# Kernel tuning notes

Measured on AMD Instinct MI355X. Metric: run time of the kernel, lower is better.

## Reference

```python
import jax, jax.numpy as jnp
import numpy as np

EPS = 1e-06
N_HEADS = 32
HEAD_DIM = 128
D_STATE = 128
D_MODEL = 2048
D_INNER = 4096
BATCH = 64


def setup_inputs() -> dict:
    key = jax.random.key(0)
    ks = jax.random.split(key, 8)
    bc_dim = N_HEADS * D_STATE
    theta_dim = N_HEADS * (D_STATE // 2)
    proj_dim = 2 * D_INNER + 2 * bc_dim + 2 * N_HEADS + theta_dim  # 18496
    x = jax.random.normal(ks[0], (BATCH, D_MODEL), jnp.float32)
    h = jax.random.normal(ks[1], (BATCH, N_HEADS, D_STATE, HEAD_DIM), jnp.float32) * 0.1
    B_prev = jax.random.normal(ks[2], (BATCH, N_HEADS, D_STATE), jnp.float32)
    x_prev = jax.random.normal(ks[3], (BATCH, N_HEADS, HEAD_DIM), jnp.float32)
    theta_cumsum = jax.random.normal(ks[4], (BATCH, N_HEADS, D_STATE // 2), jnp.float32)
    W_in = jax.random.normal(ks[5], (proj_dim, D_MODEL), jnp.float32) * 0.02
    # A_log initialized as log(arange(1, d_state+1)) repeated per head
    A_log = jnp.log(jnp.arange(1, D_STATE + 1, dtype=jnp.float32))[None, :].repeat(N_HEADS, axis=0)
    B_bias = jnp.ones((N_HEADS, D_STATE), jnp.float32)
    C_bias = jnp.ones((N_HEADS, D_STATE), jnp.float32)
    W_out = jax.random.normal(ks[6], (D_MODEL, D_INNER), jnp.float32) * 0.02
    return {"x": x, "h": h, "B_prev": B_prev, "x_prev": x_prev,
            "theta_cumsum": theta_cumsum, "W_in": W_in, "A_log": A_log,
            "B_bias": B_bias, "C_bias": C_bias, "W_out": W_out}


def _rms_norm(v):
    # RMS over last dim (v already fp32)
    rms = jnp.sqrt(jnp.mean(v * v, axis=-1, keepdims=True) + EPS)
    return v / rms


def _apply_rope(v, freqs):
    # v: (B,H,N), freqs: (B,H,N//2); interleaved pairs
    vp = v.reshape(*v.shape[:-1], -1, 2)
    c, s = jnp.cos(freqs), jnp.sin(freqs)
    v0, v1 = vp[..., 0], vp[..., 1]
    y0 = v0 * c - v1 * s
    y1 = v0 * s + v1 * c
    return jnp.stack([y0, y1], axis=-1).reshape(v.shape)


def reference(x, h, B_prev, x_prev, theta_cumsum, W_in, A_log, B_bias, C_bias, W_out):
    batch = x.shape[0]
    bc_dim = N_HEADS * D_STATE
    proj = x @ W_in.T  # (B, proj_dim)
    idx = 0
    x_proj = proj[:, idx:idx + D_INNER]; idx += D_INNER
    z = proj[:, idx:idx + D_INNER]; idx += D_INNER
    B_raw = proj[:, idx:idx + bc_dim]; idx += bc_dim
    C_raw = proj[:, idx:idx + bc_dim]; idx += bc_dim
    dt_raw = proj[:, idx:idx + N_HEADS]; idx += N_HEADS
    lam_raw = proj[:, idx:idx + N_HEADS]; idx += N_HEADS
    theta = proj[:, idx:].reshape(batch, N_HEADS, D_STATE // 2)

    x_proj = x_proj.reshape(batch, N_HEADS, HEAD_DIM)
    z = z.reshape(batch, N_HEADS, HEAD_DIM)
    B_raw = B_raw.reshape(batch, N_HEADS, D_STATE)
    C_raw = C_raw.reshape(batch, N_HEADS, D_STATE)

    B = _rms_norm(B_raw) + B_bias
    C = _rms_norm(C_raw) + C_bias

    dt = jax.nn.softplus(dt_raw)                       # (B,H)
    theta_cumsum_new = theta_cumsum + theta * dt[:, :, None]
    B = _apply_rope(B, theta_cumsum_new)
    C = _apply_rope(C, theta_cumsum_new)

    lam = jax.nn.sigmoid(lam_raw)                      # (B,H)
    A = -jnp.mean(jnp.exp(A_log), axis=-1)             # (H,)
    alpha = jnp.exp(dt * A)                            # (B,H)
    beta = (1.0 - lam) * dt * alpha
    gamma = lam * dt

    Bx_prev = jnp.einsum('bhn,bhp->bhnp', B_prev, x_prev)
    Bx_curr = jnp.einsum('bhn,bhp->bhnp', B, x_proj)
    h_new = (alpha[:, :, None, None] * h
             + beta[:, :, None, None] * Bx_prev
             + gamma[:, :, None, None] * Bx_curr)      # (B,H,N,P)

    y = jnp.einsum('bhn,bhnp->bhp', C, h_new)
    y = y * jax.nn.silu(z)
    y = y.reshape(batch, D_INNER) @ W_out.T            # (B, d_model)
    return y, h_new, B, x_proj, theta_cumsum_new
```

## Files before the change

kernel.cpp:

```cpp
#include <hip/hip_runtime.h>
#include <hip/hip_bf16.h>
#include <cstdint>
#include <cmath>

#define EPSV 1e-6f
#define PSTR 1183744

typedef __attribute__((ext_vector_type(8))) short bf16x8;
typedef __attribute__((ext_vector_type(4))) float f32x4;

typedef __attribute__((address_space(3))) unsigned int lds_u32;
typedef const __attribute__((address_space(1))) unsigned int g_u32;

__device__ __forceinline__ void load_lds16(const void* g, void* l) {
  __builtin_amdgcn_global_load_lds((g_u32*)g, (lds_u32*)l, 16, 0, 0);
}

__device__ __forceinline__ short f2b(float f) {
  unsigned u = __float_as_uint(f);
  u = (u + 0x7fffu + ((u >> 16) & 1u)) >> 16;
  return (short)u;
}

__device__ __forceinline__ bf16x8 cvt8(float4 a, float4 b) {
  bf16x8 v;
  v[0]=f2b(a.x); v[1]=f2b(a.y); v[2]=f2b(a.z); v[3]=f2b(a.w);
  v[4]=f2b(b.x); v[5]=f2b(b.y); v[6]=f2b(b.z); v[7]=f2b(b.w);
  return v;
}

__global__ __launch_bounds__(256) void conv_bf16(
    const float* __restrict__ in, short* __restrict__ out, int n8) {
  const int i = blockIdx.x * 256 + threadIdx.x;
  if (i < n8) {
    float4 a = ((const float4*)in)[2 * i];
    float4 b = ((const float4*)in)[2 * i + 1];
    ((bf16x8*)out)[i] = cvt8(a, b);
  }
}

#define GLOAD4(dst, base) \
  asm volatile("global_load_dwordx4 %0, %1, off" : "=&v"(dst) : "v"(base) : "memory")
#define GLOAD4O(dst, base, OFF) \
  asm volatile("global_load_dwordx4 %0, %1, off offset:" #OFF \
               : "=&v"(dst) : "v"(base) : "memory")

template<int KSPLIT, int NCHUNK>
__global__ __launch_bounds__(256, 4) void gemm_alds(
    const short* __restrict__ Abf, const float* __restrict__ W,
    float* __restrict__ Outp, int N, int K) {
  __shared__ short Alds[64 * 256];
  const int tid = threadIdx.x;
  const int lane = tid & 63;
  const int wv = tid >> 6;
  const int lrow = lane & 15, lk = lane >> 4;
  const int bid = blockIdx.x;
  const int ks = bid % KSPLIT;
  const int n0 = (bid / KSPLIT) * 64 + wv * 16;
  const int kbase = ks * (NCHUNK * 256);

  f32x4 acc[4];
#pragma unroll
  for (int i = 0; i < 4; ++i) acc[i] = (f32x4){0.f, 0.f, 0.f, 0.f};

  const int sr = (lane >> 5);
  const int ss = lane & 31;

  float4 wbuf[2][2];

#define WISSUE(B, CH, T) do { \
    const float* wp_ = W + (size_t)(n0 + lrow) * K + kbase + (CH) * 256 + (T) * 32 + lk * 8; \
    GLOAD4 (wbuf[B][0], wp_); \
    GLOAD4O(wbuf[B][1], wp_, 16); \
  } while (0)

#pragma unroll
  for (int ch = 0; ch < NCHUNK; ++ch) {
    __builtin_amdgcn_s_barrier();
#pragma unroll
    for (int j = 0; j < 8; ++j) {
      const int c = wv * 8 + j;
      const int r = 2 * c + sr;
      const int g = ss ^ (r & 31);
      load_lds16(Abf + (size_t)r * K + kbase + ch * 256 + g * 8,
                 (char*)Alds + c * 1024);
    }
    WISSUE(0, ch, 0);
    asm volatile("s_waitcnt vmcnt(2)" ::: "memory");
    __builtin_amdgcn_sched_barrier(0);
    __builtin_amdgcn_s_barrier();

#pragma unroll
    for (int t = 0; t < 8; ++t) {
      if (t < 7) {
        WISSUE((t + 1) & 1, ch, t + 1);
        asm volatile("s_waitcnt vmcnt(2)" ::: "memory");
      } else {
        asm volatile("s_waitcnt vmcnt(0)" ::: "memory");
      }
      __builtin_amdgcn_sched_barrier(0);
      const bf16x8 wb = cvt8(wbuf[t & 1][0], wbuf[t & 1][1]);
#pragma unroll
      for (int mf = 0; mf < 4; ++mf) {
        const int rm = mf * 16 + lrow;
        const int s = (t * 4 + lk) ^ (rm & 31);
        const bf16x8 av = *(const bf16x8*)((const char*)Alds + rm * 512 + s * 16);
        acc[mf] = __builtin_amdgcn_mfma_f32_16x16x32_bf16(av, wb, acc[mf], 0, 0, 0);
      }
    }
  }
#undef WISSUE

  float* ob = Outp + (size_t)ks * 64 * N + n0 + lrow;
#pragma unroll
  for (int mf = 0; mf < 4; ++mf)
#pragma unroll
    for (int i = 0; i < 4; ++i)
      ob[(size_t)(mf * 16 + lk * 4 + i) * N] = acc[mf][i];
}

__device__ __forceinline__ float block_reduce_sum256(float v, float* red, int t) {
#pragma unroll
  for (int o = 32; o > 0; o >>= 1) v += __shfl_xor(v, o, 64);
  __syncthreads();
  if ((t & 63) == 0) red[t >> 6] = v;
  __syncthreads();
  return red[0] + red[1] + red[2] + red[3];
}

__global__ __launch_bounds__(256) void state_update(
    const float* __restrict__ pp, const float* __restrict__ h,
    const float* __restrict__ B_prev, const float* __restrict__ x_prev,
    const float* __restrict__ theta_cumsum, const float* __restrict__ A_log,
    const float* __restrict__ B_bias, const float* __restrict__ C_bias,
    float* __restrict__ o_h, float* __restrict__ o_B,
    float* __restrict__ o_xp, float* __restrict__ o_th,
    short* __restrict__ ysbf) {
  const int bid = blockIdx.x;
  const int b = bid >> 5, hd = bid & 31;
  const int t = threadIdx.x;
  const size_t pb = (size_t)b * 18496;
#define PJ(o) (pp[pb + (o)] + pp[PSTR + pb + (o)] + pp[2 * PSTR + pb + (o)] \
             + pp[3 * PSTR + pb + (o)])

  __shared__ float sB[128], sC[128], sBp[128], sXp[128], sXv[128];
  __shared__ float red[8];
  __shared__ float yred[8][128];

  float aval = (t < 128) ? expf(A_log[hd * 128 + t]) : 0.f;
  float brv  = (t < 128) ? PJ(8192 + hd * 128 + t) : 0.f;
  float crv  = (t < 128) ? PJ(12288 + hd * 128 + t) : 0.f;
  if (t < 128) {
    sBp[t] = B_prev[(size_t)bid * 128 + t];
    float xp = PJ(hd * 128 + t);
    sXp[t] = xp;
    o_xp[(size_t)bid * 128 + t] = xp;
    sXv[t] = x_prev[(size_t)bid * 128 + t];
  }
  float sumA  = block_reduce_sum256(aval, red, t);
  float sumB2 = block_reduce_sum256(brv * brv, red, t);
  float sumC2 = block_reduce_sum256(crv * crv, red, t);

  const float dt_raw  = PJ(16384 + hd);
  const float lam_raw = PJ(16416 + hd);
  const float dt  = (dt_raw > 20.f) ? dt_raw : log1pf(expf(dt_raw));
  const float lam = 1.f / (1.f + expf(-lam_raw));
  const float A     = -sumA * (1.f / 128.f);
  const float alpha = expf(dt * A);
  const float beta  = (1.f - lam) * dt * alpha;
  const float gamma = lam * dt;
  const float rb = rsqrtf(sumB2 * (1.f / 128.f) + EPSV);
  const float rc = rsqrtf(sumC2 * (1.f / 128.f) + EPSV);

  if (t < 64) {
    float b0 = PJ(8192 + hd * 128 + 2 * t);
    float b1 = PJ(8192 + hd * 128 + 2 * t + 1);
    float c0 = PJ(12288 + hd * 128 + 2 * t);
    float c1 = PJ(12288 + hd * 128 + 2 * t + 1);
    b0 = b0 * rb + B_bias[hd * 128 + 2 * t];
    b1 = b1 * rb + B_bias[hd * 128 + 2 * t + 1];
    c0 = c0 * rc + C_bias[hd * 128 + 2 * t];
    c1 = c1 * rc + C_bias[hd * 128 + 2 * t + 1];
    const float th = theta_cumsum[(size_t)bid * 64 + t]
                   + PJ(16448 + hd * 64 + t) * dt;
    o_th[(size_t)bid * 64 + t] = th;
    const float cth = cosf(th), sth = sinf(th);
    const float nb0 = b0 * cth - b1 * sth, nb1 = b0 * sth + b1 * cth;
    const float nc0 = c0 * cth - c1 * sth, nc1 = c0 * sth + c1 * cth;
    sB[2 * t] = nb0; sB[2 * t + 1] = nb1;
    sC[2 * t] = nc0; sC[2 * t + 1] = nc1;
    o_B[(size_t)bid * 128 + 2 * t] = nb0;
    o_B[(size_t)bid * 128 + 2 * t + 1] = nb1;
  }
  __syncthreads();

  const int p4 = t & 31, nb = t >> 5;
  const float4 xp4 = *(const float4*)&sXp[p4 * 4];
  const float4 xv4 = *(const float4*)&sXv[p4 * 4];
  const size_t hbase = (size_t)bid * 16384;
  float4 ya = {0.f, 0.f, 0.f, 0.f};
  for (int n = nb; n < 128; n += 8) {
    const float4 hv = *(const float4*)&h[hbase + n * 128 + p4 * 4];
    const float cb = gamma * sB[n];
    const float cp = beta * sBp[n];
    float4 hn;
    hn.x = alpha * hv.x + cp * xv4.x + cb * xp4.x;
    hn.y = alpha * hv.y + cp * xv4.y + cb * xp4.y;
    hn.z = alpha * hv.z + cp * xv4.z + cb * xp4.z;
    hn.w = alpha * hv.w + cp * xv4.w + cb * xp4.w;
    *(float4*)&o_h[hbase + n * 128 + p4 * 4] = hn;
    const float cn = sC[n];
    ya.x += cn * hn.x; ya.y += cn * hn.y; ya.z += cn * hn.z; ya.w += cn * hn.w;
  }
  *(float4*)&yred[nb][p4 * 4] = ya;
  __syncthreads();
  if (t < 128) {
    float y = 0.f;
#pragma unroll
    for (int j = 0; j < 8; ++j) y += yred[j][t];
    const float zv = PJ(4096 + hd * 128 + t);
    const float sig = 1.f / (1.f + expf(-zv));
    ysbf[(size_t)b * 4096 + hd * 128 + t] = f2b(y * zv * sig);
  }
#undef PJ
}

__global__ __launch_bounds__(256) void reduce_y(
    const float* __restrict__ yp, float* __restrict__ y, int n4) {
  const int i = blockIdx.x * 256 + threadIdx.x;
  if (i < n4) {
    float4 s = ((const float4*)yp)[i];
#pragma unroll
    for (int k = 1; k < 16; ++k) {
      float4 t = ((const float4*)(yp + (size_t)k * 131072))[i];
      s.x += t.x; s.y += t.y; s.z += t.z; s.w += t.w;
    }
    ((float4*)y)[i] = s;
  }
}

extern "C" void kernel_launch(void* const* d_in, const int* in_sizes, int n_in,
                              void* d_out, int out_size, void* d_ws, size_t ws_size,
                              hipStream_t stream) {
  const float* x            = (const float*)d_in[0];
  const float* h            = (const float*)d_in[1];
  const float* B_prev       = (const float*)d_in[2];
  const float* x_prev       = (const float*)d_in[3];
  const float* theta_cumsum = (const float*)d_in[4];
  const float* W_in         = (const float*)d_in[5];
  const float* A_log        = (const float*)d_in[6];
  const float* B_bias       = (const float*)d_in[7];
  const float* C_bias       = (const float*)d_in[8];
  const float* W_out        = (const float*)d_in[9];

  float* out  = (float*)d_out;
  float* o_y  = out;
  float* o_h  = out + 131072;
  float* o_B  = o_h + 33554432;
  float* o_xp = o_B + 262144;
  float* o_th = o_xp + 262144;

  float* pp   = (float*)d_ws;
  float* yp   = pp;
  short* xbf  = (short*)(pp + 4 * PSTR);
  short* ysbf = xbf + 131072;

  conv_bf16<<<dim3(64), dim3(256), 0, stream>>>(x, xbf, 16384);
  gemm_alds<4, 2><<<dim3(289 * 4), dim3(256), 0, stream>>>(
      xbf, W_in, pp, 18496, 2048);
  state_update<<<dim3(2048), dim3(256), 0, stream>>>(
      pp, h, B_prev, x_prev, theta_cumsum, A_log, B_bias, C_bias,
      o_h, o_B, o_xp, o_th, ysbf);
  gemm_alds<16, 1><<<dim3(32 * 16), dim3(256), 0, stream>>>(
      ysbf, W_out, yp, 2048, 4096);
  reduce_y<<<dim3(128), dim3(256), 0, stream>>>(yp, o_y, 32768);
}
```

Measured before the change: 124.6 us.

## Stage W and A tiles through LDS with triple-buffered async pipeline

Rewrites the GEMM kernel so that both the fp32 weight tiles and the bf16 activation tiles go through LDS via global_load_lds. The K loop runs in 64-wide steps with a three-deep buffer ring and a prefetch distance of two. Previously A was loaded into LDS once per 256-wide chunk while W went straight into registers with a two-step prefetch. The aim is to keep more memory traffic in flight, since the weight stream is the main cost. In exchange LDS use per block rises, occupancy drops to 2 blocks per CU, and there is a barrier on every 64-wide K step.

```diff
diff --git a/kernel.cpp b/kernel.cpp
--- a/kernel.cpp
+++ b/kernel.cpp
@@ -39,79 +39,79 @@
   }
 }
 
-#define GLOAD4(dst, base) \
-  asm volatile("global_load_dwordx4 %0, %1, off" : "=&v"(dst) : "v"(base) : "memory")
-#define GLOAD4O(dst, base, OFF) \
-  asm volatile("global_load_dwordx4 %0, %1, off offset:" #OFF \
-               : "=&v"(dst) : "v"(base) : "memory")
-
-template<int KSPLIT, int NCHUNK>
-__global__ __launch_bounds__(256, 4) void gemm_alds(
+template<int KSPLIT, int NT>
+__global__ __launch_bounds__(256, 2) void gemm_wlds(
     const short* __restrict__ Abf, const float* __restrict__ W,
     float* __restrict__ Outp, int N, int K) {
-  __shared__ short Alds[64 * 256];
+  __shared__ float Wlds[3][64 * 64];
+  __shared__ short Alds[3][64 * 64];
   const int tid = threadIdx.x;
   const int lane = tid & 63;
   const int wv = tid >> 6;
   const int lrow = lane & 15, lk = lane >> 4;
   const int bid = blockIdx.x;
   const int ks = bid % KSPLIT;
-  const int n0 = (bid / KSPLIT) * 64 + wv * 16;
-  const int kbase = ks * (NCHUNK * 256);
+  const int nblk = (bid / KSPLIT) * 64;
+  const int kbase = ks * (NT * 64);
 
   f32x4 acc[4];
 #pragma unroll
   for (int i = 0; i < 4; ++i) acc[i] = (f32x4){0.f, 0.f, 0.f, 0.f};
 
-  const int sr = (lane >> 5);
-  const int ss = lane & 31;
-
-  float4 wbuf[2][2];
-
-#define WISSUE(B, CH, T) do { \
-    const float* wp_ = W + (size_t)(n0 + lrow) * K + kbase + (CH) * 256 + (T) * 32 + lk * 8; \
-    GLOAD4 (wbuf[B][0], wp_); \
-    GLOAD4O(wbuf[B][1], wp_, 16); \
-  } while (0)
-
-#pragma unroll
-  for (int ch = 0; ch < NCHUNK; ++ch) {
-    __builtin_amdgcn_s_barrier();
-#pragma unroll
-    for (int j = 0; j < 8; ++j) {
-      const int c = wv * 8 + j;
-      const int r = 2 * c + sr;
-      const int g = ss ^ (r & 31);
-      load_lds16(Abf + (size_t)r * K + kbase + ch * 256 + g * 8,
-                 (char*)Alds + c * 1024);
-    }
-    WISSUE(0, ch, 0);
-    asm volatile("s_waitcnt vmcnt(2)" ::: "memory");
+  auto stage = [&](int buf, int k0) {
+#pragma unroll
+    for (int j = 0; j < 4; ++j) {
+      const int c = wv * 4 + j;
+      const int r = c * 4 + (lane >> 4);
+      const int g = (lane & 15) ^ (r & 15);
+      load_lds16(W + (size_t)(nblk + r) * K + k0 + g * 4,
+                 (char*)&Wlds[buf][0] + c * 1024);
+    }
+#pragma unroll
+    for (int j = 0; j < 2; ++j) {
+      const int c = wv * 2 + j;
+      const int r = c * 8 + (lane >> 3);
+      const int g = (lane & 7) ^ (r & 7);
+      load_lds16(Abf + (size_t)r * K + k0 + g * 8,
+                 (char*)&Alds[buf][0] + c * 1024);
+    }
+  };
+
+  auto compute = [&](int buf) {
+    const int wr = wv * 16 + lrow;
+#pragma unroll
+    for (int kc = 0; kc < 2; ++kc) {
+      const int g0 = kc * 8 + lk * 2;
+      const float4 wlo = *(const float4*)((const char*)&Wlds[buf][0]
+                          + wr * 256 + ((g0 ^ (lrow & 15)) * 16));
+      const float4 whi = *(const float4*)((const char*)&Wlds[buf][0]
+                          + wr * 256 + (((g0 + 1) ^ (lrow & 15)) * 16));
+      const bf16x8 wb = cvt8(wlo, whi);
+#pragma unroll
+      for (int mf = 0; mf < 4; ++mf) {
+        const int ar = mf * 16 + lrow;
+        const int ga = ((kc << 2) | lk) ^ (ar & 7);
+        const bf16x8 av = *(const bf16x8*)((const char*)&Alds[buf][0]
+                           + ar * 128 + ga * 16);
+        acc[mf] = __builtin_amdgcn_mfma_f32_16x16x32_bf16(av, wb, acc[mf], 0, 0, 0);
+      }
+    }
+  };
+
+  stage(0, kbase);
+  stage(1, kbase + 64);
+
+  for (int t = 0; t < NT; ++t) {
+    if (t < NT - 1) asm volatile("s_waitcnt vmcnt(6)" ::: "memory");
+    else            asm volatile("s_waitcnt vmcnt(0)" ::: "memory");
     __builtin_amdgcn_sched_barrier(0);
     __builtin_amdgcn_s_barrier();
-
-#pragma unroll
-    for (int t = 0; t < 8; ++t) {
-      if (t < 7) {
-        WISSUE((t + 1) & 1, ch, t + 1);
-        asm volatile("s_waitcnt vmcnt(2)" ::: "memory");
-      } else {
-        asm volatile("s_waitcnt vmcnt(0)" ::: "memory");
-      }
-      __builtin_amdgcn_sched_barrier(0);
-      const bf16x8 wb = cvt8(wbuf[t & 1][0], wbuf[t & 1][1]);
-#pragma unroll
-      for (int mf = 0; mf < 4; ++mf) {
-        const int rm = mf * 16 + lrow;
-        const int s = (t * 4 + lk) ^ (rm & 31);
-        const bf16x8 av = *(const bf16x8*)((const char*)Alds + rm * 512 + s * 16);
-        acc[mf] = __builtin_amdgcn_mfma_f32_16x16x32_bf16(av, wb, acc[mf], 0, 0, 0);
-      }
-    }
-  }
-#undef WISSUE
-
-  float* ob = Outp + (size_t)ks * 64 * N + n0 + lrow;
+    __builtin_amdgcn_sched_barrier(0);
+    compute(t % 3);
+    if (t + 2 <= NT - 1) stage((t + 2) % 3, kbase + (t + 2) * 64);
+  }
+
+  float* ob = Outp + (size_t)ks * 64 * N + nblk + wv * 16 + lrow;
 #pragma unroll
   for (int mf = 0; mf < 4; ++mf)
 #pragma unroll
@@ -266,12 +266,12 @@
   short* ysbf = xbf + 131072;
 
   conv_bf16<<<dim3(64), dim3(256), 0, stream>>>(x, xbf, 16384);
-  gemm_alds<4, 2><<<dim3(289 * 4), dim3(256), 0, stream>>>(
+  gemm_wlds<4, 8><<<dim3(289 * 4), dim3(256), 0, stream>>>(
       xbf, W_in, pp, 18496, 2048);
   state_update<<<dim3(2048), dim3(256), 0, stream>>>(
       pp, h, B_prev, x_prev, theta_cumsum, A_log, B_bias, C_bias,
       o_h, o_B, o_xp, o_th, ysbf);
-  gemm_alds<16, 1><<<dim3(32 * 16), dim3(256), 0, stream>>>(
+  gemm_wlds<16, 4><<<dim3(32 * 16), dim3(256), 0, stream>>>(
       ysbf, W_out, yp, 2048, 4096);
   reduce_y<<<dim3(128), dim3(256), 0, stream>>>(yp, o_y, 32768);
 }
```

New measurement: 121.1 us. 2.8% less time.
